# Performance work log

Hardware: AMD Instinct MI355X
Metric: run time of the kernel (lower is better)

Reference implementation:

```python
import jax, jax.numpy as jnp
import numpy as np

N = 2048        # batch (nodes/edges)
DIM = 512       # irreps dim for x, y, and output
C = 16          # channel multiplicity
NNZ = 4096      # number of sparse CG paths


def setup_inputs() -> dict:
    key = jax.random.key(0)
    k1, k2, k3, k4, k5, k6 = jax.random.split(key, 6)
    x = jax.random.normal(k1, (N, DIM, C), dtype=jnp.float32)
    y = jax.random.normal(k2, (N, DIM, C), dtype=jnp.float32)
    scale = jax.random.normal(k3, (NNZ,), dtype=jnp.float32)
    index1 = jax.random.randint(k4, (NNZ,), 0, DIM)
    index2 = jax.random.randint(k5, (NNZ,), 0, DIM)
    index_out = jnp.sort(jax.random.randint(k6, (NNZ,), 0, DIM))
    return {"x": x, "y": y, "scale": scale,
            "index1": index1, "index2": index2, "index_out": index_out,
            "out_size": DIM}


def reference(x, y, scale, index1, index2, index_out, out_size):
    # gather both operands along the irreps dim  -> [N, NNZ, C]
    inter = scale[None, :, None] * x[:, index1, :] * y[:, index2, :]
    # scatter-add (segment + scatter in the original, fused here since
    # segment-then-scatter over disjoint segments == one scatter-add)
    out = jnp.zeros((x.shape[0], out_size, x.shape[-1]), dtype=x.dtype)
    out = out.at[:, index_out, :].add(inter)  # [N, out_size, C]
    return out
```

## Files before the change

kernel.cpp:

```cpp
#include <hip/hip_runtime.h>

constexpr int DIM = 512;
constexpr int C   = 16;
constexpr int TPB = 1024;
constexpr int STRIDE = 20;
constexpr int LDSF = DIM * STRIDE;

__global__ __launch_bounds__(1024) void setup_kernel(
    const int* __restrict__ io,
    const int* __restrict__ i1,
    const int* __restrict__ i2,
    const float* __restrict__ scale,
    int4* __restrict__ plan,
    int4* __restrict__ pdata,
    int nnz) {
    if (blockIdx.x == 0) {
        __shared__ int s_start[DIM + 1];
        __shared__ int s_len[DIM];
        const int t = threadIdx.x;
        if (t <= DIM) {
            int lo = 0, hi = nnz;
            while (lo < hi) {
                int mid = (lo + hi) >> 1;
                if (io[mid] < t) lo = mid + 1; else hi = mid;
            }
            s_start[t] = lo;
        }
        __syncthreads();
        if (t < DIM) s_len[t] = s_start[t + 1] - s_start[t];
        __syncthreads();
        if (t < DIM) {
            const int ld = s_len[t];
            int rank = 0;
            #pragma unroll 8
            for (int j = 0; j < DIM; ++j) {
                const int lj = s_len[j];
                rank += (lj > ld) || (lj == ld && j < t);
            }
            plan[rank] = make_int4(s_start[t], s_start[t + 1], t * C, 0);
        }
    } else {
        const int p = (blockIdx.x - 1) * 1024 + threadIdx.x;
        if (p < nnz)
            pdata[p] = make_int4(i1[p] * STRIDE, i2[p] * STRIDE,
                                 __float_as_int(scale[p]), 0);
    }
}

__global__ __launch_bounds__(TPB) void tp_kernel(
    const float* __restrict__ x, const float* __restrict__ y,
    const int4* __restrict__ plan,
    const int4* __restrict__ pdata,
    float* __restrict__ out) {
    extern __shared__ float lds[];
    float* xs = lds;
    float* ys = lds + LDSF;
    float4* xs4 = reinterpret_cast<float4*>(xs);
    float4* ys4 = reinterpret_cast<float4*>(ys);

    const int n = blockIdx.x;
    const float4* __restrict__ xg = reinterpret_cast<const float4*>(x) + (size_t)n * (DIM * C / 4);
    const float4* __restrict__ yg = reinterpret_cast<const float4*>(y) + (size_t)n * (DIM * C / 4);

    const int l4  = threadIdx.x & 3;
    const int grp = threadIdx.x >> 2;
    const int c4f = l4 * 4;

    const int4 plA = plan[grp];
    const int4 plB = plan[DIM - 1 - grp];
    const int sA = plA.x, eA = plA.y, lastA = eA - 1;
    const int sB = plB.x, eB = plB.y, lastB = eB - 1;
    int4 qA0, qA1, qB0, qB1;
    if (sA < eA) {
        qA0 = pdata[sA];
        qA1 = pdata[sA + 1 < lastA ? sA + 1 : lastA];
    }
    if (sB < eB) {
        qB0 = pdata[sB];
        qB1 = pdata[sB + 1 < lastB ? sB + 1 : lastB];
    }

    #pragma unroll
    for (int s = threadIdx.x; s < DIM * 4; s += TPB) {
        const int slot = (s >> 2) * 5 + (s & 3);
        xs4[slot] = xg[s];
        ys4[slot] = yg[s];
    }
    __syncthreads();

    float* __restrict__ obase = out + (size_t)n * (DIM * C) + c4f;

    float aAx = 0.f, aAy = 0.f, aAz = 0.f, aAw = 0.f;
    if (sA < eA) {
        float4 v0x = *reinterpret_cast<const float4*>(xs + qA0.x + c4f);
        float4 v0y = *reinterpret_cast<const float4*>(ys + qA0.y + c4f);
        float4 v1x = *reinterpret_cast<const float4*>(xs + qA1.x + c4f);
        float4 v1y = *reinterpret_cast<const float4*>(ys + qA1.y + c4f);
        float s0 = __int_as_float(qA0.z);
        float s1 = __int_as_float(qA1.z);
        int4 q2 = pdata[sA + 2 < lastA ? sA + 2 : lastA];
        int4 q3 = pdata[sA + 3 < lastA ? sA + 3 : lastA];
        for (int p = sA; p < eA; ++p) {
            const int4 q4 = pdata[p + 4 < lastA ? p + 4 : lastA];
            const float4 v2x = *reinterpret_cast<const float4*>(xs + q2.x + c4f);
            const float4 v2y = *reinterpret_cast<const float4*>(ys + q2.y + c4f);
            aAx = fmaf(s0 * v0x.x, v0y.x, aAx);
            aAy = fmaf(s0 * v0x.y, v0y.y, aAy);
            aAz = fmaf(s0 * v0x.z, v0y.z, aAz);
            aAw = fmaf(s0 * v0x.w, v0y.w, aAw);
            s0 = s1; s1 = __int_as_float(q2.z);
            q2 = q3; q3 = q4;
            v0x = v1x; v0y = v1y; v1x = v2x; v1y = v2y;
        }
    }

    float4 w0x, w0y, w1x, w1y;
    int4 r2, r3;
    float t0 = 0.f, t1 = 0.f;
    if (sB < eB) {
        w0x = *reinterpret_cast<const float4*>(xs + qB0.x + c4f);
        w0y = *reinterpret_cast<const float4*>(ys + qB0.y + c4f);
        w1x = *reinterpret_cast<const float4*>(xs + qB1.x + c4f);
        w1y = *reinterpret_cast<const float4*>(ys + qB1.y + c4f);
        t0 = __int_as_float(qB0.z);
        t1 = __int_as_float(qB1.z);
        r2 = pdata[sB + 2 < lastB ? sB + 2 : lastB];
        r3 = pdata[sB + 3 < lastB ? sB + 3 : lastB];
    }

    *reinterpret_cast<float4*>(obase + plA.z) = make_float4(aAx, aAy, aAz, aAw);

    float aBx = 0.f, aBy = 0.f, aBz = 0.f, aBw = 0.f;
    if (sB < eB) {
        for (int p = sB; p < eB; ++p) {
            const int4 r4 = pdata[p + 4 < lastB ? p + 4 : lastB];
            const float4 v2x = *reinterpret_cast<const float4*>(xs + r2.x + c4f);
            const float4 v2y = *reinterpret_cast<const float4*>(ys + r2.y + c4f);
            aBx = fmaf(t0 * w0x.x, w0y.x, aBx);
            aBy = fmaf(t0 * w0x.y, w0y.y, aBy);
            aBz = fmaf(t0 * w0x.z, w0y.z, aBz);
            aBw = fmaf(t0 * w0x.w, w0y.w, aBw);
            t0 = t1; t1 = __int_as_float(r2.z);
            r2 = r3; r3 = r4;
            w0x = w1x; w0y = w1y; w1x = v2x; w1y = v2y;
        }
    }
    *reinterpret_cast<float4*>(obase + plB.z) = make_float4(aBx, aBy, aBz, aBw);
}

extern "C" void kernel_launch(void* const* d_in, const int* in_sizes, int n_in,
                              void* d_out, int out_size, void* d_ws, size_t ws_size,
                              hipStream_t stream) {
    const float* x     = (const float*)d_in[0];
    const float* y     = (const float*)d_in[1];
    const float* scale = (const float*)d_in[2];
    const int*   i1    = (const int*)d_in[3];
    const int*   i2    = (const int*)d_in[4];
    const int*   io    = (const int*)d_in[5];
    float* out = (float*)d_out;

    const int nnz = in_sizes[2];
    const int N   = in_sizes[0] / (DIM * C);

    int4* plan  = (int4*)d_ws;
    int4* pdata = (int4*)((char*)d_ws + 8192);

    const int pack_blocks = (nnz + 1023) / 1024;
    setup_kernel<<<1 + pack_blocks, 1024, 0, stream>>>(io, i1, i2, scale, plan, pdata, nnz);

    constexpr size_t lds_bytes = (size_t)2 * LDSF * sizeof(float);
    (void)hipFuncSetAttribute((const void*)tp_kernel,
                              hipFuncAttributeMaxDynamicSharedMemorySize,
                              (int)lds_bytes);
    tp_kernel<<<N, TPB, lds_bytes, stream>>>(x, y, plan, pdata, out);
}
```

Before: 80.30 us.

## Make tp_kernel persistent with double-buffered LDS prefetch of next batch row

Launches a fixed 256 blocks that loop over batch elements, prefetching the next element's x/y into registers while computing the current one, then storing into an alternate LDS buffer. Plan and index metadata are loaded once per block instead of per element. This doubles LDS usage per block, which limits residency to one block per CU, and adds a block-wide barrier per element.

After: 74.31 us. -7.4%, faster.

```diff
diff --git a/kernel.cpp b/kernel.cpp
--- a/kernel.cpp
+++ b/kernel.cpp
@@ -4,7 +4,8 @@
 constexpr int C   = 16;
 constexpr int TPB = 1024;
 constexpr int STRIDE = 20;
-constexpr int LDSF = DIM * STRIDE;
+constexpr int BUF = DIM * STRIDE;
+constexpr int NBLK = 256;
 
 __global__ __launch_bounds__(1024) void setup_kernel(
     const int* __restrict__ io,
@@ -51,17 +52,11 @@
     const float* __restrict__ x, const float* __restrict__ y,
     const int4* __restrict__ plan,
     const int4* __restrict__ pdata,
-    float* __restrict__ out) {
+    float* __restrict__ out,
+    int N) {
     extern __shared__ float lds[];
-    float* xs = lds;
-    float* ys = lds + LDSF;
-    float4* xs4 = reinterpret_cast<float4*>(xs);
-    float4* ys4 = reinterpret_cast<float4*>(ys);
 
-    const int n = blockIdx.x;
-    const float4* __restrict__ xg = reinterpret_cast<const float4*>(x) + (size_t)n * (DIM * C / 4);
-    const float4* __restrict__ yg = reinterpret_cast<const float4*>(y) + (size_t)n * (DIM * C / 4);
-
+    const int nb  = blockIdx.x;
     const int l4  = threadIdx.x & 3;
     const int grp = threadIdx.x >> 2;
     const int c4f = l4 * 4;
@@ -80,72 +75,99 @@
         qB1 = pdata[sB + 1 < lastB ? sB + 1 : lastB];
     }
 
-    #pragma unroll
-    for (int s = threadIdx.x; s < DIM * 4; s += TPB) {
-        const int slot = (s >> 2) * 5 + (s & 3);
-        xs4[slot] = xg[s];
-        ys4[slot] = yg[s];
+    const float4* __restrict__ xg = reinterpret_cast<const float4*>(x);
+    const float4* __restrict__ yg = reinterpret_cast<const float4*>(y);
+    const int t0 = threadIdx.x;
+    const int t1 = threadIdx.x + TPB;
+    const int slot0 = (t0 >> 2) * 5 + (t0 & 3);
+    const int slot1 = (t1 >> 2) * 5 + (t1 & 3);
+
+    if (nb < N) {
+        const size_t gb = (size_t)nb * (DIM * C / 4);
+        const float4 a0 = xg[gb + t0], a1 = xg[gb + t1];
+        const float4 b0 = yg[gb + t0], b1 = yg[gb + t1];
+        float4* xs4 = reinterpret_cast<float4*>(lds);
+        float4* ys4 = reinterpret_cast<float4*>(lds + BUF);
+        xs4[slot0] = a0; xs4[slot1] = a1;
+        ys4[slot0] = b0; ys4[slot1] = b1;
     }
     __syncthreads();
 
-    float* __restrict__ obase = out + (size_t)n * (DIM * C) + c4f;
+    int k = 0;
+    for (int n = nb; n < N; n += NBLK) {
+        float* xs = lds + k * (2 * BUF);
+        float* ys = xs + BUF;
 
-    float aAx = 0.f, aAy = 0.f, aAz = 0.f, aAw = 0.f;
-    if (sA < eA) {
-        float4 v0x = *reinterpret_cast<const float4*>(xs + qA0.x + c4f);
-        float4 v0y = *reinterpret_cast<const float4*>(ys + qA0.y + c4f);
-        float4 v1x = *reinterpret_cast<const float4*>(xs + qA1.x + c4f);
-        float4 v1y = *reinterpret_cast<const float4*>(ys + qA1.y + c4f);
-        float s0 = __int_as_float(qA0.z);
-        float s1 = __int_as_float(qA1.z);
-        int4 q2 = pdata[sA + 2 < lastA ? sA + 2 : lastA];
-        int4 q3 = pdata[sA + 3 < lastA ? sA + 3 : lastA];
-        for (int p = sA; p < eA; ++p) {
-            const int4 q4 = pdata[p + 4 < lastA ? p + 4 : lastA];
-            const float4 v2x = *reinterpret_cast<const float4*>(xs + q2.x + c4f);
-            const float4 v2y = *reinterpret_cast<const float4*>(ys + q2.y + c4f);
-            aAx = fmaf(s0 * v0x.x, v0y.x, aAx);
-            aAy = fmaf(s0 * v0x.y, v0y.y, aAy);
-            aAz = fmaf(s0 * v0x.z, v0y.z, aAz);
-            aAw = fmaf(s0 * v0x.w, v0y.w, aAw);
-            s0 = s1; s1 = __int_as_float(q2.z);
-            q2 = q3; q3 = q4;
-            v0x = v1x; v0y = v1y; v1x = v2x; v1y = v2y;
+        const bool more = (n + NBLK) < N;
+        float4 a0, a1, b0, b1;
+        if (more) {
+            const size_t gb = (size_t)(n + NBLK) * (DIM * C / 4);
+            a0 = xg[gb + t0]; a1 = xg[gb + t1];
+            b0 = yg[gb + t0]; b1 = yg[gb + t1];
         }
+
+        float aAx = 0.f, aAy = 0.f, aAz = 0.f, aAw = 0.f;
+        if (sA < eA) {
+            float4 v0x = *reinterpret_cast<const float4*>(xs + qA0.x + c4f);
+            float4 v0y = *reinterpret_cast<const float4*>(ys + qA0.y + c4f);
+            float4 v1x = *reinterpret_cast<const float4*>(xs + qA1.x + c4f);
+            float4 v1y = *reinterpret_cast<const float4*>(ys + qA1.y + c4f);
+            float s0 = __int_as_float(qA0.z);
+            float s1 = __int_as_float(qA1.z);
+            int4 q2 = pdata[sA + 2 < lastA ? sA + 2 : lastA];
+            int4 q3 = pdata[sA + 3 < lastA ? sA + 3 : lastA];
+            for (int p = sA; p < eA; ++p) {
+                const int4 q4 = pdata[p + 4 < lastA ? p + 4 : lastA];
+                const float4 v2x = *reinterpret_cast<const float4*>(xs + q2.x + c4f);
+                const float4 v2y = *reinterpret_cast<const float4*>(ys + q2.y + c4f);
+                aAx = fmaf(s0 * v0x.x, v0y.x, aAx);
+                aAy = fmaf(s0 * v0x.y, v0y.y, aAy);
+                aAz = fmaf(s0 * v0x.z, v0y.z, aAz);
+                aAw = fmaf(s0 * v0x.w, v0y.w, aAw);
+                s0 = s1; s1 = __int_as_float(q2.z);
+                q2 = q3; q3 = q4;
+                v0x = v1x; v0y = v1y; v1x = v2x; v1y = v2y;
+            }
+        }
+
+        float aBx = 0.f, aBy = 0.f, aBz = 0.f, aBw = 0.f;
+        if (sB < eB) {
+            float4 w0x = *reinterpret_cast<const float4*>(xs + qB0.x + c4f);
+            float4 w0y = *reinterpret_cast<const float4*>(ys + qB0.y + c4f);
+            float4 w1x = *reinterpret_cast<const float4*>(xs + qB1.x + c4f);
+            float4 w1y = *reinterpret_cast<const float4*>(ys + qB1.y + c4f);
+            float t0s = __int_as_float(qB0.z);
+            float t1s = __int_as_float(qB1.z);
+            int4 r2 = pdata[sB + 2 < lastB ? sB + 2 : lastB];
+            int4 r3 = pdata[sB + 3 < lastB ? sB + 3 : lastB];
+            for (int p = sB; p < eB; ++p) {
+                const int4 r4 = pdata[p + 4 < lastB ? p + 4 : lastB];
+                const float4 v2x = *reinterpret_cast<const float4*>(xs + r2.x + c4f);
+                const float4 v2y = *reinterpret_cast<const float4*>(ys + r2.y + c4f);
+                aBx = fmaf(t0s * w0x.x, w0y.x, aBx);
+                aBy = fmaf(t0s * w0x.y, w0y.y, aBy);
+                aBz = fmaf(t0s * w0x.z, w0y.z, aBz);
+                aBw = fmaf(t0s * w0x.w, w0y.w, aBw);
+                t0s = t1s; t1s = __int_as_float(r2.z);
+                r2 = r3; r3 = r4;
+                w0x = w1x; w0y = w1y; w1x = v2x; w1y = v2y;
+            }
+        }
+
+        if (more) {
+            float* nbuf = lds + (k ^ 1) * (2 * BUF);
+            float4* nx4 = reinterpret_cast<float4*>(nbuf);
+            float4* ny4 = reinterpret_cast<float4*>(nbuf + BUF);
+            nx4[slot0] = a0; nx4[slot1] = a1;
+            ny4[slot0] = b0; ny4[slot1] = b1;
+        }
+
+        float* obase = out + (size_t)n * (DIM * C) + c4f;
+        *reinterpret_cast<float4*>(obase + plA.z) = make_float4(aAx, aAy, aAz, aAw);
+        *reinterpret_cast<float4*>(obase + plB.z) = make_float4(aBx, aBy, aBz, aBw);
+        __syncthreads();
+        k ^= 1;
     }
-
-    float4 w0x, w0y, w1x, w1y;
-    int4 r2, r3;
-    float t0 = 0.f, t1 = 0.f;
-    if (sB < eB) {
-        w0x = *reinterpret_cast<const float4*>(xs + qB0.x + c4f);
-        w0y = *reinterpret_cast<const float4*>(ys + qB0.y + c4f);
-        w1x = *reinterpret_cast<const float4*>(xs + qB1.x + c4f);
-        w1y = *reinterpret_cast<const float4*>(ys + qB1.y + c4f);
-        t0 = __int_as_float(qB0.z);
-        t1 = __int_as_float(qB1.z);
-        r2 = pdata[sB + 2 < lastB ? sB + 2 : lastB];
-        r3 = pdata[sB + 3 < lastB ? sB + 3 : lastB];
-    }
-
-    *reinterpret_cast<float4*>(obase + plA.z) = make_float4(aAx, aAy, aAz, aAw);
-
-    float aBx = 0.f, aBy = 0.f, aBz = 0.f, aBw = 0.f;
-    if (sB < eB) {
-        for (int p = sB; p < eB; ++p) {
-            const int4 r4 = pdata[p + 4 < lastB ? p + 4 : lastB];
-            const float4 v2x = *reinterpret_cast<const float4*>(xs + r2.x + c4f);
-            const float4 v2y = *reinterpret_cast<const float4*>(ys + r2.y + c4f);
-            aBx = fmaf(t0 * w0x.x, w0y.x, aBx);
-            aBy = fmaf(t0 * w0x.y, w0y.y, aBy);
-            aBz = fmaf(t0 * w0x.z, w0y.z, aBz);
-            aBw = fmaf(t0 * w0x.w, w0y.w, aBw);
-            t0 = t1; t1 = __int_as_float(r2.z);
-            r2 = r3; r3 = r4;
-            w0x = w1x; w0y = w1y; w1x = v2x; w1y = v2y;
-        }
-    }
-    *reinterpret_cast<float4*>(obase + plB.z) = make_float4(aBx, aBy, aBz, aBw);
 }
 
 extern "C" void kernel_launch(void* const* d_in, const int* in_sizes, int n_in,
@@ -168,9 +190,9 @@
     const int pack_blocks = (nnz + 1023) / 1024;
     setup_kernel<<<1 + pack_blocks, 1024, 0, stream>>>(io, i1, i2, scale, plan, pdata, nnz);
 
-    constexpr size_t lds_bytes = (size_t)2 * LDSF * sizeof(float);
+    constexpr size_t lds_bytes = (size_t)4 * BUF * sizeof(float);
     (void)hipFuncSetAttribute((const void*)tp_kernel,
                               hipFuncAttributeMaxDynamicSharedMemorySize,
                               (int)lds_bytes);
-    tp_kernel<<<N, TPB, lds_bytes, stream>>>(x, y, plan, pdata, out);
+    tp_kernel<<<NBLK, TPB, lds_bytes, stream>>>(x, y, plan, pdata, out, N);
 }
```
